# Kernel tuning notes

Measured on AMD Instinct MI355X. Metric: run time of the kernel, lower is better.

The kernel has to match this reference:

```python
import jax, jax.numpy as jnp
import numpy as np

B = 4
N0, N1, N2 = 32768, 8192, 2048
C0, C1, C2 = 256, 512, 1024
EPS = 1e-5  # torch BatchNorm1d default eps


def _mlp(x, w1, b1, g, be, w2, b2):
    # Linear -> BatchNorm1d (training-mode batch stats over B and N) -> ReLU -> Linear
    h = x @ w1 + b1                      # (B, N, H)
    mu = jnp.mean(h, axis=(0, 1))
    var = jnp.mean((h - mu) ** 2, axis=(0, 1))  # biased var, as torch BN uses for normalization
    h = jax.nn.relu((h - mu) * jax.lax.rsqrt(var + EPS) * g + be)
    return h @ w2 + b2


def _gather(feats, idx):
    # feats: (B, N_coarse, C), idx: (B, N_fine) -> (B, N_fine, C)
    return jax.vmap(lambda f, i: f[i])(feats, idx)


def _lin(key, fan_in, fan_out, scale=0.02):
    return jax.random.normal(key, (fan_in, fan_out), dtype=jnp.float32) * scale


def setup_inputs() -> dict:
    key = jax.random.key(0)
    ks = jax.random.split(key, 16)
    inp = {
        'f0': jax.random.normal(ks[0], (B, N0, C0), dtype=jnp.float32),
        'f1': jax.random.normal(ks[1], (B, N1, C1), dtype=jnp.float32),
        'f2': jax.random.normal(ks[2], (B, N2, C2), dtype=jnp.float32),
        # up_mlps[0]: MLP(C1, [C1, C0])
        'up0_w1': _lin(ks[3], C1, C1), 'up0_b1': jnp.zeros((C1,), jnp.float32),
        'up0_g': jnp.ones((C1,), jnp.float32), 'up0_be': jnp.zeros((C1,), jnp.float32),
        'up0_w2': _lin(ks[4], C1, C0), 'up0_b2': jnp.zeros((C0,), jnp.float32),
        # up_mlps[1]: MLP(C2, [C2, C1])
        'up1_w1': _lin(ks[5], C2, C2), 'up1_b1': jnp.zeros((C2,), jnp.float32),
        'up1_g': jnp.ones((C2,), jnp.float32), 'up1_be': jnp.zeros((C2,), jnp.float32),
        'up1_w2': _lin(ks[6], C2, C1), 'up1_b2': jnp.zeros((C1,), jnp.float32),
        # skip_mlps[0]: MLP(2*C0, [2*C0, C0])
        'skip0_w1': _lin(ks[7], 2 * C0, 2 * C0), 'skip0_b1': jnp.zeros((2 * C0,), jnp.float32),
        'skip0_g': jnp.ones((2 * C0,), jnp.float32), 'skip0_be': jnp.zeros((2 * C0,), jnp.float32),
        'skip0_w2': _lin(ks[8], 2 * C0, C0), 'skip0_b2': jnp.zeros((C0,), jnp.float32),
        # skip_mlps[1]: MLP(2*C1, [2*C1, C1])
        'skip1_w1': _lin(ks[9], 2 * C1, 2 * C1), 'skip1_b1': jnp.zeros((2 * C1,), jnp.float32),
        'skip1_g': jnp.ones((2 * C1,), jnp.float32), 'skip1_be': jnp.zeros((2 * C1,), jnp.float32),
        'skip1_w2': _lin(ks[10], 2 * C1, C1), 'skip1_b2': jnp.zeros((C1,), jnp.float32),
        'pool0': jax.random.randint(ks[11], (B, N0), 0, N1, dtype=jnp.int32),
        'pool1': jax.random.randint(ks[12], (B, N1), 0, N2, dtype=jnp.int32),
    }
    return inp


def reference(f0, f1, f2,
              up0_w1, up0_b1, up0_g, up0_be, up0_w2, up0_b2,
              up1_w1, up1_b1, up1_g, up1_be, up1_w2, up1_b2,
              skip0_w1, skip0_b1, skip0_g, skip0_be, skip0_w2, skip0_b2,
              skip1_w1, skip1_b1, skip1_g, skip1_be, skip1_w2, skip1_b2,
              pool0, pool1):
    # start at coarsest level
    x = f2                                               # (B, N2, C2)
    # level i = 1
    x = _mlp(x, up1_w1, up1_b1, up1_g, up1_be, up1_w2, up1_b2)   # (B, N2, C1)
    x = _gather(x, pool1)                                 # (B, N1, C1)
    x = _mlp(jnp.concatenate([f1, x], axis=-1),
             skip1_w1, skip1_b1, skip1_g, skip1_be, skip1_w2, skip1_b2)  # (B, N1, C1)
    # level i = 0
    x = _mlp(x, up0_w1, up0_b1, up0_g, up0_be, up0_w2, up0_b2)   # (B, N1, C0)
    x = _gather(x, pool0)                                 # (B, N0, C0)
    x = _mlp(jnp.concatenate([f0, x], axis=-1),
             skip0_w1, skip0_b1, skip0_g, skip0_be, skip0_w2, skip0_b2)  # (B, N0, C0)
    return x
```

## Files before the change

### kernel.cpp

```cpp
#include <hip/hip_runtime.h>


typedef unsigned short u16;
typedef __attribute__((ext_vector_type(8))) short bf16x8;
typedef __attribute__((ext_vector_type(4))) float f32x4;

#define UNROLL _Pragma("unroll")
#define EPW 264

__device__ __forceinline__ float b2f(u16 u) {
    union { unsigned int i; float f; } v; v.i = ((unsigned int)u) << 16; return v.f;
}
__device__ __forceinline__ u16 f2b(float f) {
    union { float f; unsigned int i; } v; v.f = f;
    unsigned int r = v.i + 0x7FFFu + ((v.i >> 16) & 1u);
    return (u16)(r >> 16);
}

__device__ __forceinline__ void gld_lds16(const u16* g, u16* l) {
    __builtin_amdgcn_global_load_lds(
        (const __attribute__((address_space(1))) unsigned int*)g,
        (__attribute__((address_space(3))) unsigned int*)l,
        16, 0, 0);
}

#define VMCNT(n) asm volatile("s_waitcnt vmcnt(" #n ")" ::: "memory")
#define LGKM0    asm volatile("s_waitcnt lgkmcnt(0)" ::: "memory")
#define BAR()    do{ asm volatile("" ::: "memory"); \
                     __builtin_amdgcn_s_barrier(); \
                     asm volatile("" ::: "memory"); }while(0)

union SMem {
    struct { u16 a[3][16384]; u16 b[16384]; } g;
    struct { u16 a[2][16384]; u16 b[2][16384]; float ss[2048]; } f;
    u16 ep[256 * EPW];
};

template <bool AFFINE_A, bool STATS, bool OUT_F32, bool GATHER>
__global__ __launch_bounds__(512, 2) void gemm_bn(
    const u16* __restrict__ A, const u16* __restrict__ BT, void* __restrict__ Cout,
    const float* __restrict__ scale, const float* __restrict__ shift,
    const float* __restrict__ bias,
    float* __restrict__ psum, float* __restrict__ psumsq,
    const u16* __restrict__ Xg, const int* __restrict__ pool,
    int nfShift, int Nc, int Chalf,
    int N, int K)
{
    __shared__ __align__(16) SMem sm;

    const int tid  = threadIdx.x;
    const int w    = tid >> 6;
    const int lane = tid & 63;
    const int wm   = w >> 2, wn = w & 3;
    const int l15  = lane & 15;
    const int xorv = (lane & 7) << 3;
    const int swz8 = ((lane & 7) ^ (lane >> 3)) << 3;
    const int kS0  = (((lane >> 4) << 3)) ^ xorv;
    const int kS1  = (32 + ((lane >> 4) << 3)) ^ xorv;

    int bm, bn;
    {
        const int nbn  = (int)gridDim.x;
        const int nwg  = nbn * (int)gridDim.y;
        const int flat = (int)(blockIdx.y * gridDim.x + blockIdx.x);
        const int wg   = (flat & 7) * (nwg >> 3) + (flat >> 3);
        const int lb   = 31 - __builtin_clz(nbn);
        bn = wg & (nbn - 1);
        bm = wg >> lb;
    }

    const u16* aS[2][2]; const u16* xS[2][2]; const u16* bS[2][2];
    int dA[2][2], dB[2][2], wIdx[2][2];
    UNROLL for (int u = 0; u < 2; u++)
    UNROLL for (int ld = 0; ld < 2; ld++) {
        const int urb = w * 16 + ld * 8;
        const int ur  = urb + (lane >> 3);
        {
            const int trb = urb + (urb >= 64 ? 64 : 0) + u * 64;
            const int tr  = ur  + (ur  >= 64 ? 64 : 0) + u * 64;
            dA[u][ld] = trb * 64;
            const int rowG = bm * 256 + tr;
            if constexpr (GATHER) {
                const int b = rowG >> nfShift;
                const int p = pool[rowG];
                aS[u][ld] = A  + (size_t)rowG * Chalf + swz8;
                xS[u][ld] = Xg + ((size_t)b * Nc + p) * Chalf + swz8;
            } else if constexpr (AFFINE_A) {
                aS[u][ld] = A + (size_t)rowG * K + ((lane & 7) << 3);
                wIdx[u][ld] = tr * 64 + swz8;
            } else {
                aS[u][ld] = A + (size_t)rowG * K + swz8;
            }
        }
        {
            const int trb = ((urb >> 5) << 6) + (urb & 31) + u * 32;
            const int tr  = ((ur  >> 5) << 6) + (ur  & 31) + u * 32;
            dB[u][ld] = trb * 64;
            bS[u][ld] = BT + (size_t)(bn * 256 + tr) * K + swz8;
        }
    }

    f32x4 acc[8][4];
    const f32x4 zero = {0.f, 0.f, 0.f, 0.f};
    UNROLL for (int i = 0; i < 8; i++)
    UNROLL for (int j = 0; j < 4; j++) acc[i][j] = zero;
    bf16x8 afr[4][2];
    bf16x8 bfr[2][2][2];
    uint4 rA[2][2];

#define GLD_B(u, BASE, KOF) do{ \
    u16* bt_ = (BASE); \
    gld_lds16(bS[u][0] + (KOF), bt_ + dB[u][0]); \
    gld_lds16(bS[u][1] + (KOF), bt_ + dB[u][1]); }while(0)

#define ISSUE_A(u, BASE, KOF) do{ \
    u16* at_ = (BASE); \
    if constexpr (GATHER) { \
        const u16 *s0_, *s1_; \
        if ((KOF) < Chalf) { s0_ = aS[u][0] + (KOF); s1_ = aS[u][1] + (KOF); } \
        else { s0_ = xS[u][0] + ((KOF) - Chalf); s1_ = xS[u][1] + ((KOF) - Chalf); } \
        gld_lds16(s0_, at_ + dA[u][0]); \
        gld_lds16(s1_, at_ + dA[u][1]); \
    } else { \
        gld_lds16(aS[u][0] + (KOF), at_ + dA[u][0]); \
        gld_lds16(aS[u][1] + (KOF), at_ + dA[u][1]); \
    } }while(0)

#define LOAD_RA(u, KOF) do{ \
    rA[u][0] = *(const uint4*)(aS[u][0] + (KOF)); \
    rA[u][1] = *(const uint4*)(aS[u][1] + (KOF)); }while(0)

#define AFFW(u, BASE, KOF) do{ if constexpr (AFFINE_A) { \
    u16* at_ = (BASE); \
    const int kb_ = (KOF) + ((lane & 7) << 3); \
    const float4 sc0_ = *(const float4*)&sm.f.ss[kb_]; \
    const float4 sc1_ = *(const float4*)&sm.f.ss[kb_ + 4]; \
    const float4 sh0_ = *(const float4*)&sm.f.ss[1024 + kb_]; \
    const float4 sh1_ = *(const float4*)&sm.f.ss[1024 + kb_ + 4]; \
    UNROLL for (int ld_ = 0; ld_ < 2; ld_++) { \
        union { uint4 u4; u16 s[8]; } r_, o_; r_.u4 = rA[u][ld_]; \
        o_.s[0] = f2b(fmaxf(b2f(r_.s[0]) * sc0_.x + sh0_.x, 0.f)); \
        o_.s[1] = f2b(fmaxf(b2f(r_.s[1]) * sc0_.y + sh0_.y, 0.f)); \
        o_.s[2] = f2b(fmaxf(b2f(r_.s[2]) * sc0_.z + sh0_.z, 0.f)); \
        o_.s[3] = f2b(fmaxf(b2f(r_.s[3]) * sc0_.w + sh0_.w, 0.f)); \
        o_.s[4] = f2b(fmaxf(b2f(r_.s[4]) * sc1_.x + sh1_.x, 0.f)); \
        o_.s[5] = f2b(fmaxf(b2f(r_.s[5]) * sc1_.y + sh1_.y, 0.f)); \
        o_.s[6] = f2b(fmaxf(b2f(r_.s[6]) * sc1_.z + sh1_.z, 0.f)); \
        o_.s[7] = f2b(fmaxf(b2f(r_.s[7]) * sc1_.w + sh1_.w, 0.f)); \
        *(uint4*)&at_[wIdx[u][ld_]] = o_.u4; } \
    LGKM0; } }while(0)

#define READ_A(base, qi) do{ const u16* p_ = (base); \
    UNROLL for (int i_ = 0; i_ < 4; i_++) { \
        const int rb_ = (wm * 128 + ((qi) * 4 + i_) * 16 + l15) * 64; \
        afr[i_][0] = *(const bf16x8*)&p_[rb_ + kS0]; \
        afr[i_][1] = *(const bf16x8*)&p_[rb_ + kS1]; } }while(0)

#define READ_B(base, qj) do{ const u16* p_ = (base); \
    UNROLL for (int j_ = 0; j_ < 2; j_++) { \
        const int rb_ = (wn * 64 + ((qj) * 2 + j_) * 16 + l15) * 64; \
        bfr[qj][j_][0] = *(const bf16x8*)&p_[rb_ + kS0]; \
        bfr[qj][j_][1] = *(const bf16x8*)&p_[rb_ + kS1]; } }while(0)

#define MFMA_Q(qi, qj) do{ __builtin_amdgcn_s_setprio(1); \
    UNROLL for (int i_ = 0; i_ < 4; i_++) \
    UNROLL for (int j_ = 0; j_ < 2; j_++) { \
        acc[(qi)*4+i_][(qj)*2+j_] = __builtin_amdgcn_mfma_f32_16x16x32_bf16( \
            afr[i_][0], bfr[qj][j_][0], acc[(qi)*4+i_][(qj)*2+j_], 0, 0, 0); \
        acc[(qi)*4+i_][(qj)*2+j_] = __builtin_amdgcn_mfma_f32_16x16x32_bf16( \
            afr[i_][1], bfr[qj][j_][1], acc[(qi)*4+i_][(qj)*2+j_], 0, 0, 0); } \
    __builtin_amdgcn_s_setprio(0); }while(0)

    const int nkt = K >> 6;

    if constexpr (AFFINE_A) {
        for (int i = tid; i < K; i += 512) {
            sm.f.ss[i] = scale[i]; sm.f.ss[1024 + i] = shift[i];
        }
        LOAD_RA(0, 0);
        GLD_B(0, &sm.f.b[0][0], 0); GLD_B(1, &sm.f.b[0][0], 0);
        LOAD_RA(1, 0);
        asm volatile("s_waitcnt vmcnt(0) lgkmcnt(0)" ::: "memory");
        BAR();
        AFFW(0, &sm.f.a[0][0], 0);
        BAR();

        for (int t = 0; t < nkt - 1; ++t) {
            const int buf = t & 1, nb = buf ^ 1;
            const int kofN = (t + 1) << 6;
            u16* aB = &sm.f.a[buf][0]; u16* aN = &sm.f.a[nb][0];
            u16* bB = &sm.f.b[buf][0]; u16* bN = &sm.f.b[nb][0];
            LOAD_RA(0, kofN);
            READ_A(aB, 0); READ_B(bB, 0);
            BAR();
            MFMA_Q(0, 0);
            GLD_B(0, bN, kofN);
            VMCNT(6); BAR();
            READ_B(bB, 1);
            MFMA_Q(0, 1);
            GLD_B(1, bN, kofN);
            VMCNT(6);
            AFFW(1, aB, t << 6);
            BAR();
            READ_A(aB, 1);
            MFMA_Q(1, 1);
            LOAD_RA(1, kofN);
            MFMA_Q(1, 0);
            VMCNT(4);
            AFFW(0, aN, kofN);
            BAR();
        }
        {
            const int t = nkt - 1, buf = t & 1;
            u16* aB = &sm.f.a[buf][0]; u16* bB = &sm.f.b[buf][0];
            READ_A(aB, 0); READ_B(bB, 0);
            BAR();
            MFMA_Q(0, 0);
            VMCNT(2); BAR();
            READ_B(bB, 1);
            MFMA_Q(0, 1);
            VMCNT(0);
            AFFW(1, aB, t << 6);
            BAR();
            READ_A(aB, 1);
            MFMA_Q(1, 1);
            BAR();
            MFMA_Q(1, 0);
        }
    } else {
        u16* const bb = &sm.g.b[0];
        GLD_B(0, bb, 0); GLD_B(1, bb, 0);
        ISSUE_A(0, &sm.g.a[0][0], 0);  ISSUE_A(1, &sm.g.a[0][0], 0);
        ISSUE_A(0, &sm.g.a[1][0], 64); ISSUE_A(1, &sm.g.a[1][0], 64);
        VMCNT(0); BAR();

        int rs = 0;
        for (int t = 0; t < nkt - 2; ++t) {
            const int ws = (rs == 0) ? 2 : rs - 1;
            const int kofB = (t + 1) << 6, kofL = (t + 2) << 6;
            const u16* aR = &sm.g.a[0][0] + rs * 16384;
            u16* aW = &sm.g.a[0][0] + ws * 16384;
            READ_A(aR, 0); READ_B(bb, 0);
            LGKM0; VMCNT(4); BAR();
            GLD_B(0, bb, kofB);
            MFMA_Q(0, 0);
            READ_B(bb, 1);
            LGKM0; BAR();
            GLD_B(1, bb, kofB);
            MFMA_Q(0, 1);
            READ_A(aR, 1);
            ISSUE_A(0, aW, kofL);
            BAR();
            MFMA_Q(1, 1);
            ISSUE_A(1, aW, kofL);
            MFMA_Q(1, 0);
            VMCNT(6); BAR();
            rs = (rs == 2) ? 0 : rs + 1;
        }
        {
            const int t = nkt - 2;
            const int kofB = (t + 1) << 6;
            const u16* aR = &sm.g.a[0][0] + rs * 16384;
            READ_A(aR, 0); READ_B(bb, 0);
            LGKM0; VMCNT(4); BAR();
            GLD_B(0, bb, kofB);
            MFMA_Q(0, 0);
            READ_B(bb, 1);
            LGKM0; BAR();
            GLD_B(1, bb, kofB);
            MFMA_Q(0, 1);
            READ_A(aR, 1);
            BAR();
            MFMA_Q(1, 1);
            MFMA_Q(1, 0);
            VMCNT(2); BAR();
            rs = (rs == 2) ? 0 : rs + 1;
        }
        {
            const u16* aR = &sm.g.a[0][0] + rs * 16384;
            READ_A(aR, 0); READ_B(bb, 0);
            VMCNT(0); BAR();
            MFMA_Q(0, 0);
            READ_B(bb, 1);
            MFMA_Q(0, 1);
            READ_A(aR, 1);
            MFMA_Q(1, 1);
            MFMA_Q(1, 0);
            LGKM0; BAR();
        }
    }

    const int cl = l15, quad = lane >> 4;
    if constexpr (OUT_F32) {
        UNROLL for (int j = 0; j < 4; j++) {
            const int col = bn * 256 + wn * 64 + j * 16 + cl;
            const float bcol = bias[col];
            UNROLL for (int i = 0; i < 8; i++) {
                const int r0 = bm * 256 + wm * 128 + i * 16 + quad * 4;
                UNROLL for (int r = 0; r < 4; r++)
                    ((float*)Cout)[(size_t)(r0 + r) * N + col] = acc[i][j][r] + bcol;
            }
        }
    } else {
        UNROLL for (int j = 0; j < 4; j++) {
            const int colL = wn * 64 + j * 16 + cl;
            const int col = bn * 256 + colL;
            float bcol = 0.f;
            if constexpr (!STATS) bcol = bias[col];
            float s = 0.f, ss2 = 0.f;
            UNROLL for (int i = 0; i < 8; i++) {
                const int rL0 = wm * 128 + i * 16 + quad * 4;
                UNROLL for (int r = 0; r < 4; r++) {
                    const float v = acc[i][j][r];
                    if constexpr (STATS) { s += v; ss2 += v * v; }
                    sm.ep[(rL0 + r) * EPW + colL] = f2b(v + bcol);
                }
            }
            if constexpr (STATS) {
                s   += __shfl_xor(s, 16);   s   += __shfl_xor(s, 32);
                ss2 += __shfl_xor(ss2, 16); ss2 += __shfl_xor(ss2, 32);
                if (quad == 0) { atomicAdd(&psum[col], s); atomicAdd(&psumsq[col], ss2); }
            }
        }
        __syncthreads();
        u16* Cb = (u16*)Cout;
        UNROLL for (int it = 0; it < 16; it++) {
            const int row = it * 16 + (tid >> 5);
            const int c8  = (tid & 31) * 8;
            const uint4 v = *(const uint4*)&sm.ep[row * EPW + c8];
            *(uint4*)(Cb + (size_t)(bm * 256 + row) * N + bn * 256 + c8) = v;
        }
    }
#undef GLD_B
#undef ISSUE_A
#undef LOAD_RA
#undef AFFW
#undef READ_A
#undef READ_B
#undef MFMA_Q
}

__global__ void cvt_transpose_w(const float* __restrict__ W, u16* __restrict__ WT, int K, int N) {
    __shared__ float t[32][33];
    const int tx = threadIdx.x, ty = threadIdx.y;
    const int n0 = blockIdx.x * 32, k0 = blockIdx.y * 32;
#pragma unroll
    for (int r = 0; r < 4; r++)
        t[ty + r * 8][tx] = W[(size_t)(k0 + ty + r * 8) * N + n0 + tx];
    __syncthreads();
#pragma unroll
    for (int r = 0; r < 4; r++)
        WT[(size_t)(n0 + ty + r * 8) * K + k0 + tx] = f2b(t[tx][ty + r * 8]);
}

__global__ void cvt_f32_bf16(const float* __restrict__ x, u16* __restrict__ y, long n8) {
    const long t = (long)blockIdx.x * 256 + threadIdx.x;
    if (t >= n8) return;
    const float4 a = ((const float4*)x)[t * 2];
    const float4 b = ((const float4*)x)[t * 2 + 1];
    union { uint4 u; u16 s[8]; } o;
    o.s[0] = f2b(a.x); o.s[1] = f2b(a.y); o.s[2] = f2b(a.z); o.s[3] = f2b(a.w);
    o.s[4] = f2b(b.x); o.s[5] = f2b(b.y); o.s[6] = f2b(b.z); o.s[7] = f2b(b.w);
    ((uint4*)y)[t] = o.u;
}

__global__ void bn_finalize(const float* __restrict__ sum, const float* __restrict__ sumsq,
                            const float* __restrict__ g, const float* __restrict__ be,
                            float* __restrict__ scale, float* __restrict__ shift,
                            int Cc, float invM) {
    const int c = blockIdx.x * 256 + threadIdx.x;
    if (c >= Cc) return;
    const float mu = sum[c] * invM;
    const float var = fmaf(sumsq[c], invM, -mu * mu);
    const float sc = g[c] * rsqrtf(var + 1e-5f);
    scale[c] = sc;
    shift[c] = fmaf(-mu, sc, be[c]);
}

extern "C" void kernel_launch(void* const* d_in, const int* in_sizes, int n_in,
                              void* d_out, int out_size, void* d_ws, size_t ws_size,
                              hipStream_t stream) {
    const float* f0     = (const float*)d_in[0];
    const float* f1     = (const float*)d_in[1];
    const float* f2     = (const float*)d_in[2];
    const float* up0_w1 = (const float*)d_in[3];
    const float* up0_g  = (const float*)d_in[5];
    const float* up0_be = (const float*)d_in[6];
    const float* up0_w2 = (const float*)d_in[7];
    const float* up0_b2 = (const float*)d_in[8];
    const float* up1_w1 = (const float*)d_in[9];
    const float* up1_g  = (const float*)d_in[11];
    const float* up1_be = (const float*)d_in[12];
    const float* up1_w2 = (const float*)d_in[13];
    const float* up1_b2 = (const float*)d_in[14];
    const float* sk0_w1 = (const float*)d_in[15];
    const float* sk0_g  = (const float*)d_in[17];
    const float* sk0_be = (const float*)d_in[18];
    const float* sk0_w2 = (const float*)d_in[19];
    const float* sk0_b2 = (const float*)d_in[20];
    const float* sk1_w1 = (const float*)d_in[21];
    const float* sk1_g  = (const float*)d_in[23];
    const float* sk1_be = (const float*)d_in[24];
    const float* sk1_w2 = (const float*)d_in[25];
    const float* sk1_b2 = (const float*)d_in[26];
    const int* pool0    = (const int*)d_in[27];
    const int* pool1    = (const int*)d_in[28];
    float* out = (float*)d_out;

    char* ws = (char*)d_ws;
    size_t off = 0;
    auto alloc = [&](size_t bytes) -> void* {
        void* p = ws + off;
        off += (bytes + 255) & ~(size_t)255;
        return p;
    };
    u16* w_up1_1 = (u16*)alloc((size_t)1024 * 1024 * 2);
    u16* w_up1_2 = (u16*)alloc((size_t)512 * 1024 * 2);
    u16* w_sk1_1 = (u16*)alloc((size_t)1024 * 1024 * 2);
    u16* w_sk1_2 = (u16*)alloc((size_t)512 * 1024 * 2);
    u16* w_up0_1 = (u16*)alloc((size_t)512 * 512 * 2);
    u16* w_up0_2 = (u16*)alloc((size_t)256 * 512 * 2);
    u16* w_sk0_1 = (u16*)alloc((size_t)512 * 512 * 2);
    u16* w_sk0_2 = (u16*)alloc((size_t)256 * 512 * 2);
    float* stats = (float*)alloc((size_t)4 * 4096 * 4);
    u16* Hbuf    = (u16*)alloc((size_t)131072 * 512 * 2);
    u16* Xbuf    = (u16*)alloc((size_t)32768 * 512 * 2);
    u16* f0b     = (u16*)alloc((size_t)4 * 32768 * 256 * 2);
    u16* f1b     = (u16*)alloc((size_t)4 * 8192 * 512 * 2);
    u16* f2b_    = (u16*)alloc((size_t)4 * 2048 * 1024 * 2);

    const dim3 tb(32, 8);
    cvt_transpose_w<<<dim3(32, 32), tb, 0, stream>>>(up1_w1, w_up1_1, 1024, 1024);
    cvt_transpose_w<<<dim3(16, 32), tb, 0, stream>>>(up1_w2, w_up1_2, 1024, 512);
    cvt_transpose_w<<<dim3(32, 32), tb, 0, stream>>>(sk1_w1, w_sk1_1, 1024, 1024);
    cvt_transpose_w<<<dim3(16, 32), tb, 0, stream>>>(sk1_w2, w_sk1_2, 1024, 512);
    cvt_transpose_w<<<dim3(16, 16), tb, 0, stream>>>(up0_w1, w_up0_1, 512, 512);
    cvt_transpose_w<<<dim3(8, 16),  tb, 0, stream>>>(up0_w2, w_up0_2, 512, 256);
    cvt_transpose_w<<<dim3(16, 16), tb, 0, stream>>>(sk0_w1, w_sk0_1, 512, 512);
    cvt_transpose_w<<<dim3(8, 16),  tb, 0, stream>>>(sk0_w2, w_sk0_2, 512, 256);

    hipMemsetAsync(stats, 0, (size_t)4 * 4096 * sizeof(float), stream);
    cvt_f32_bf16<<<4096,  256, 0, stream>>>(f2, f2b_, 8388608L / 8);
    cvt_f32_bf16<<<8192,  256, 0, stream>>>(f1, f1b, 16777216L / 8);
    cvt_f32_bf16<<<16384, 256, 0, stream>>>(f0, f0b, 33554432L / 8);

    float* st0 = stats;
    float* st1 = stats + 4096;
    float* st2 = stats + 8192;
    float* st3 = stats + 12288;

    gemm_bn<false, true, false, false><<<dim3(4, 32), 512, 0, stream>>>(
        f2b_, w_up1_1, Hbuf, nullptr, nullptr, nullptr, st0, st0 + 1024,
        nullptr, nullptr, 0, 0, 0, 1024, 1024);
    bn_finalize<<<4, 256, 0, stream>>>(st0, st0 + 1024, up1_g, up1_be, st0 + 2048, st0 + 3072, 1024, 1.f / 8192.f);
    gemm_bn<true, false, false, false><<<dim3(2, 32), 512, 0, stream>>>(
        Hbuf, w_up1_2, Xbuf, st0 + 2048, st0 + 3072, up1_b2, nullptr, nullptr,
        nullptr, nullptr, 0, 0, 0, 512, 1024);

    gemm_bn<false, true, false, true><<<dim3(4, 128), 512, 0, stream>>>(
        f1b, w_sk1_1, Hbuf, nullptr, nullptr, nullptr, st1, st1 + 1024,
        Xbuf, pool1, 13, 2048, 512, 1024, 1024);
    bn_finalize<<<4, 256, 0, stream>>>(st1, st1 + 1024, sk1_g, sk1_be, st1 + 2048, st1 + 3072, 1024, 1.f / 32768.f);
    gemm_bn<true, false, false, false><<<dim3(2, 128), 512, 0, stream>>>(
        Hbuf, w_sk1_2, Xbuf, st1 + 2048, st1 + 3072, sk1_b2, nullptr, nullptr,
        nullptr, nullptr, 0, 0, 0, 512, 1024);

    gemm_bn<false, true, false, false><<<dim3(2, 128), 512, 0, stream>>>(
        Xbuf, w_up0_1, Hbuf, nullptr, nullptr, nullptr, st2, st2 + 1024,
        nullptr, nullptr, 0, 0, 0, 512, 512);
    bn_finalize<<<2, 256, 0, stream>>>(st2, st2 + 1024, up0_g, up0_be, st2 + 2048, st2 + 3072, 512, 1.f / 32768.f);
    gemm_bn<true, false, false, false><<<dim3(1, 128), 512, 0, stream>>>(
        Hbuf, w_up0_2, Xbuf, st2 + 2048, st2 + 3072, up0_b2, nullptr, nullptr,
        nullptr, nullptr, 0, 0, 0, 256, 512);

    gemm_bn<false, true, false, true><<<dim3(2, 512), 512, 0, stream>>>(
        f0b, w_sk0_1, Hbuf, nullptr, nullptr, nullptr, st3, st3 + 1024,
        Xbuf, pool0, 15, 8192, 256, 512, 512);
    bn_finalize<<<2, 256, 0, stream>>>(st3, st3 + 1024, sk0_g, sk0_be, st3 + 2048, st3 + 3072, 512, 1.f / 131072.f);
    gemm_bn<true, false, true, false><<<dim3(1, 512), 512, 0, stream>>>(
        Hbuf, w_sk0_2, out, st3 + 2048, st3 + 3072, sk0_b2, nullptr, nullptr,
        nullptr, nullptr, 0, 0, 0, 256, 512);
}
```

Measured before the change: 833.4 us.

## Shrink GEMM tile to 256x128 with 1024-thread blocks and double-buffered B

Blocks now cover a 256x128 output tile with 16 waves of 64x32 each instead of 256x256 with 8 waves, and launch 1024 threads with double the grid along N. B tiles become double-buffered at half size and the K-loop pipeline is restructured into two MFMA phases per step. The aim is more blocks and waves to hide latency and better CU fill on the small-N GEMMs. The cost is lower arithmetic intensity per tile, more redundant A traffic and more barriers per K-step. Launch bounds (1024,4) also cap registers hard.

Result: slower. 850.8 us (+2.1%).

```diff
diff --git a/kernel.cpp b/kernel.cpp
--- a/kernel.cpp
+++ b/kernel.cpp
@@ -6,7 +6,7 @@
 typedef __attribute__((ext_vector_type(4))) float f32x4;
 
 #define UNROLL _Pragma("unroll")
-#define EPW 264
+#define EPW 136
 
 __device__ __forceinline__ float b2f(u16 u) {
     union { unsigned int i; float f; } v; v.i = ((unsigned int)u) << 16; return v.f;
@@ -31,13 +31,13 @@
                      asm volatile("" ::: "memory"); }while(0)
 
 union SMem {
-    struct { u16 a[3][16384]; u16 b[16384]; } g;
-    struct { u16 a[2][16384]; u16 b[2][16384]; float ss[2048]; } f;
+    struct { u16 a[3][16384]; u16 b[2][8192]; } g;
+    struct { u16 a[2][16384]; u16 b[2][8192]; float ss[2048]; } f;
     u16 ep[256 * EPW];
 };
 
 template <bool AFFINE_A, bool STATS, bool OUT_F32, bool GATHER>
-__global__ __launch_bounds__(512, 2) void gemm_bn(
+__global__ __launch_bounds__(1024, 4) void gemm_bn(
     const u16* __restrict__ A, const u16* __restrict__ BT, void* __restrict__ Cout,
     const float* __restrict__ scale, const float* __restrict__ shift,
     const float* __restrict__ bias,
@@ -55,7 +55,7 @@
     const int l15  = lane & 15;
     const int xorv = (lane & 7) << 3;
     const int swz8 = ((lane & 7) ^ (lane >> 3)) << 3;
-    const int kS0  = (((lane >> 4) << 3)) ^ xorv;
+    const int kS0  = ((lane >> 4) << 3) ^ xorv;
     const int kS1  = (32 + ((lane >> 4) << 3)) ^ xorv;
 
     int bm, bn;
@@ -69,247 +69,219 @@
         bm = wg >> lb;
     }
 
-    const u16* aS[2][2]; const u16* xS[2][2]; const u16* bS[2][2];
-    int dA[2][2], dB[2][2], wIdx[2][2];
-    UNROLL for (int u = 0; u < 2; u++)
-    UNROLL for (int ld = 0; ld < 2; ld++) {
-        const int urb = w * 16 + ld * 8;
-        const int ur  = urb + (lane >> 3);
-        {
-            const int trb = urb + (urb >= 64 ? 64 : 0) + u * 64;
-            const int tr  = ur  + (ur  >= 64 ? 64 : 0) + u * 64;
-            dA[u][ld] = trb * 64;
-            const int rowG = bm * 256 + tr;
-            if constexpr (GATHER) {
-                const int b = rowG >> nfShift;
-                const int p = pool[rowG];
-                aS[u][ld] = A  + (size_t)rowG * Chalf + swz8;
-                xS[u][ld] = Xg + ((size_t)b * Nc + p) * Chalf + swz8;
-            } else if constexpr (AFFINE_A) {
-                aS[u][ld] = A + (size_t)rowG * K + ((lane & 7) << 3);
-                wIdx[u][ld] = tr * 64 + swz8;
-            } else {
-                aS[u][ld] = A + (size_t)rowG * K + swz8;
-            }
-        }
-        {
-            const int trb = ((urb >> 5) << 6) + (urb & 31) + u * 32;
-            const int tr  = ((ur  >> 5) << 6) + (ur  & 31) + u * 32;
-            dB[u][ld] = trb * 64;
-            bS[u][ld] = BT + (size_t)(bn * 256 + tr) * K + swz8;
+    const u16* aS[2]; const u16* xS[2]; const u16* bSp;
+    int dA[2], dB, wIdx[2];
+    UNROLL for (int u = 0; u < 2; u++) {
+        const int trb = (w >> 2) * 64 + (w & 3) * 8 + u * 32;
+        const int tr  = trb + (lane >> 3);
+        dA[u] = trb * 64;
+        const int rowG = bm * 256 + tr;
+        if constexpr (GATHER) {
+            const int b = rowG >> nfShift;
+            const int p = pool[rowG];
+            aS[u] = A  + (size_t)rowG * Chalf + swz8;
+            xS[u] = Xg + ((size_t)b * Nc + p) * Chalf + swz8;
+        } else if constexpr (AFFINE_A) {
+            aS[u] = A + (size_t)rowG * K + ((lane & 7) << 3);
+            wIdx[u] = tr * 64 + swz8;
+        } else {
+            aS[u] = A + (size_t)rowG * K + swz8;
         }
     }
-
-    f32x4 acc[8][4];
+    {
+        const int trb = w * 8;
+        dB = trb * 64;
+        bSp = BT + (size_t)(bn * 128 + trb + (lane >> 3)) * K + swz8;
+    }
+
+    f32x4 acc[4][2];
     const f32x4 zero = {0.f, 0.f, 0.f, 0.f};
-    UNROLL for (int i = 0; i < 8; i++)
-    UNROLL for (int j = 0; j < 4; j++) acc[i][j] = zero;
-    bf16x8 afr[4][2];
-    bf16x8 bfr[2][2][2];
-    uint4 rA[2][2];
-
-#define GLD_B(u, BASE, KOF) do{ \
-    u16* bt_ = (BASE); \
-    gld_lds16(bS[u][0] + (KOF), bt_ + dB[u][0]); \
-    gld_lds16(bS[u][1] + (KOF), bt_ + dB[u][1]); }while(0)
+    UNROLL for (int i = 0; i < 4; i++)
+    UNROLL for (int j = 0; j < 2; j++) acc[i][j] = zero;
+    bf16x8 afr[2][2];
+    bf16x8 bfr[2][2];
+    uint4 rA[2];
+
+#define GLD_B(BASE, KOF) gld_lds16(bSp + (KOF), (BASE) + dB)
 
 #define ISSUE_A(u, BASE, KOF) do{ \
-    u16* at_ = (BASE); \
     if constexpr (GATHER) { \
-        const u16 *s0_, *s1_; \
-        if ((KOF) < Chalf) { s0_ = aS[u][0] + (KOF); s1_ = aS[u][1] + (KOF); } \
-        else { s0_ = xS[u][0] + ((KOF) - Chalf); s1_ = xS[u][1] + ((KOF) - Chalf); } \
-        gld_lds16(s0_, at_ + dA[u][0]); \
-        gld_lds16(s1_, at_ + dA[u][1]); \
+        const u16* s_ = ((KOF) < Chalf) ? (aS[u] + (KOF)) : (xS[u] + ((KOF) - Chalf)); \
+        gld_lds16(s_, (BASE) + dA[u]); \
     } else { \
-        gld_lds16(aS[u][0] + (KOF), at_ + dA[u][0]); \
-        gld_lds16(aS[u][1] + (KOF), at_ + dA[u][1]); \
+        gld_lds16(aS[u] + (KOF), (BASE) + dA[u]); \
     } }while(0)
 
-#define LOAD_RA(u, KOF) do{ \
-    rA[u][0] = *(const uint4*)(aS[u][0] + (KOF)); \
-    rA[u][1] = *(const uint4*)(aS[u][1] + (KOF)); }while(0)
+#define LOAD_RA(u, KOF) do{ rA[u] = *(const uint4*)(aS[u] + (KOF)); }while(0)
 
 #define AFFW(u, BASE, KOF) do{ if constexpr (AFFINE_A) { \
-    u16* at_ = (BASE); \
     const int kb_ = (KOF) + ((lane & 7) << 3); \
     const float4 sc0_ = *(const float4*)&sm.f.ss[kb_]; \
     const float4 sc1_ = *(const float4*)&sm.f.ss[kb_ + 4]; \
     const float4 sh0_ = *(const float4*)&sm.f.ss[1024 + kb_]; \
     const float4 sh1_ = *(const float4*)&sm.f.ss[1024 + kb_ + 4]; \
-    UNROLL for (int ld_ = 0; ld_ < 2; ld_++) { \
-        union { uint4 u4; u16 s[8]; } r_, o_; r_.u4 = rA[u][ld_]; \
-        o_.s[0] = f2b(fmaxf(b2f(r_.s[0]) * sc0_.x + sh0_.x, 0.f)); \
-        o_.s[1] = f2b(fmaxf(b2f(r_.s[1]) * sc0_.y + sh0_.y, 0.f)); \
-        o_.s[2] = f2b(fmaxf(b2f(r_.s[2]) * sc0_.z + sh0_.z, 0.f)); \
-        o_.s[3] = f2b(fmaxf(b2f(r_.s[3]) * sc0_.w + sh0_.w, 0.f)); \
-        o_.s[4] = f2b(fmaxf(b2f(r_.s[4]) * sc1_.x + sh1_.x, 0.f)); \
-        o_.s[5] = f2b(fmaxf(b2f(r_.s[5]) * sc1_.y + sh1_.y, 0.f)); \
-        o_.s[6] = f2b(fmaxf(b2f(r_.s[6]) * sc1_.z + sh1_.z, 0.f)); \
-        o_.s[7] = f2b(fmaxf(b2f(r_.s[7]) * sc1_.w + sh1_.w, 0.f)); \
-        *(uint4*)&at_[wIdx[u][ld_]] = o_.u4; } \
+    union { uint4 u4; u16 s[8]; } r_, o_; r_.u4 = rA[u]; \
+    o_.s[0] = f2b(fmaxf(b2f(r_.s[0]) * sc0_.x + sh0_.x, 0.f)); \
+    o_.s[1] = f2b(fmaxf(b2f(r_.s[1]) * sc0_.y + sh0_.y, 0.f)); \
+    o_.s[2] = f2b(fmaxf(b2f(r_.s[2]) * sc0_.z + sh0_.z, 0.f)); \
+    o_.s[3] = f2b(fmaxf(b2f(r_.s[3]) * sc0_.w + sh0_.w, 0.f)); \
+    o_.s[4] = f2b(fmaxf(b2f(r_.s[4]) * sc1_.x + sh1_.x, 0.f)); \
+    o_.s[5] = f2b(fmaxf(b2f(r_.s[5]) * sc1_.y + sh1_.y, 0.f)); \
+    o_.s[6] = f2b(fmaxf(b2f(r_.s[6]) * sc1_.z + sh1_.z, 0.f)); \
+    o_.s[7] = f2b(fmaxf(b2f(r_.s[7]) * sc1_.w + sh1_.w, 0.f)); \
+    *(uint4*)&((BASE))[wIdx[u]] = o_.u4; \
     LGKM0; } }while(0)
 
 #define READ_A(base, qi) do{ const u16* p_ = (base); \
-    UNROLL for (int i_ = 0; i_ < 4; i_++) { \
-        const int rb_ = (wm * 128 + ((qi) * 4 + i_) * 16 + l15) * 64; \
-        afr[i_][0] = *(const bf16x8*)&p_[rb_ + kS0]; \
-        afr[i_][1] = *(const bf16x8*)&p_[rb_ + kS1]; } }while(0)
-
-#define READ_B(base, qj) do{ const u16* p_ = (base); \
+    UNROLL for (int i2 = 0; i2 < 2; i2++) { \
+        const int rb_ = (wm * 64 + ((qi) * 2 + i2) * 16 + l15) * 64; \
+        afr[i2][0] = *(const bf16x8*)&p_[rb_ + kS0]; \
+        afr[i2][1] = *(const bf16x8*)&p_[rb_ + kS1]; } }while(0)
+
+#define READ_B(base) do{ const u16* p_ = (base); \
     UNROLL for (int j_ = 0; j_ < 2; j_++) { \
-        const int rb_ = (wn * 64 + ((qj) * 2 + j_) * 16 + l15) * 64; \
-        bfr[qj][j_][0] = *(const bf16x8*)&p_[rb_ + kS0]; \
-        bfr[qj][j_][1] = *(const bf16x8*)&p_[rb_ + kS1]; } }while(0)
-
-#define MFMA_Q(qi, qj) do{ __builtin_amdgcn_s_setprio(1); \
-    UNROLL for (int i_ = 0; i_ < 4; i_++) \
+        const int rb_ = (wn * 32 + j_ * 16 + l15) * 64; \
+        bfr[j_][0] = *(const bf16x8*)&p_[rb_ + kS0]; \
+        bfr[j_][1] = *(const bf16x8*)&p_[rb_ + kS1]; } }while(0)
+
+#define MFMA_PH(qi) do{ __builtin_amdgcn_s_setprio(1); \
+    UNROLL for (int i2 = 0; i2 < 2; i2++) \
     UNROLL for (int j_ = 0; j_ < 2; j_++) { \
-        acc[(qi)*4+i_][(qj)*2+j_] = __builtin_amdgcn_mfma_f32_16x16x32_bf16( \
-            afr[i_][0], bfr[qj][j_][0], acc[(qi)*4+i_][(qj)*2+j_], 0, 0, 0); \
-        acc[(qi)*4+i_][(qj)*2+j_] = __builtin_amdgcn_mfma_f32_16x16x32_bf16( \
-            afr[i_][1], bfr[qj][j_][1], acc[(qi)*4+i_][(qj)*2+j_], 0, 0, 0); } \
+        acc[(qi)*2+i2][j_] = __builtin_amdgcn_mfma_f32_16x16x32_bf16( \
+            afr[i2][0], bfr[j_][0], acc[(qi)*2+i2][j_], 0, 0, 0); \
+        acc[(qi)*2+i2][j_] = __builtin_amdgcn_mfma_f32_16x16x32_bf16( \
+            afr[i2][1], bfr[j_][1], acc[(qi)*2+i2][j_], 0, 0, 0); } \
     __builtin_amdgcn_s_setprio(0); }while(0)
 
     const int nkt = K >> 6;
 
     if constexpr (AFFINE_A) {
-        for (int i = tid; i < K; i += 512) {
+        for (int i = tid; i < K; i += 1024) {
             sm.f.ss[i] = scale[i]; sm.f.ss[1024 + i] = shift[i];
         }
-        LOAD_RA(0, 0);
-        GLD_B(0, &sm.f.b[0][0], 0); GLD_B(1, &sm.f.b[0][0], 0);
-        LOAD_RA(1, 0);
-        asm volatile("s_waitcnt vmcnt(0) lgkmcnt(0)" ::: "memory");
+        LOAD_RA(0, 0); LOAD_RA(1, 0);
+        GLD_B(&sm.f.b[0][0], 0);
+        GLD_B(&sm.f.b[1][0], 64);
+        LGKM0;
         BAR();
         AFFW(0, &sm.f.a[0][0], 0);
+        LOAD_RA(0, 64);
+        VMCNT(2);
         BAR();
 
-        for (int t = 0; t < nkt - 1; ++t) {
-            const int buf = t & 1, nb = buf ^ 1;
+        for (int t = 0; t < nkt - 2; ++t) {
+            u16* aB = &sm.f.a[t & 1][0]; u16* aN = &sm.f.a[(t + 1) & 1][0];
+            u16* bR = &sm.f.b[t & 1][0];
+            const int kofN = (t + 1) << 6, kof2 = (t + 2) << 6;
+            AFFW(1, aB, t << 6);
+            LOAD_RA(1, kofN);
+            READ_A(aB, 0); READ_B(bR);
+            LGKM0; BAR();
+            MFMA_PH(0);
+            AFFW(0, aN, kofN);
+            LOAD_RA(0, kof2);
+            GLD_B(bR, kof2);
+            READ_A(aB, 1);
+            LGKM0; VMCNT(3);
+            BAR();
+            MFMA_PH(1);
+        }
+        {
+            const int t = nkt - 2;
+            u16* aB = &sm.f.a[t & 1][0]; u16* aN = &sm.f.a[(t + 1) & 1][0];
+            u16* bR = &sm.f.b[t & 1][0];
             const int kofN = (t + 1) << 6;
-            u16* aB = &sm.f.a[buf][0]; u16* aN = &sm.f.a[nb][0];
-            u16* bB = &sm.f.b[buf][0]; u16* bN = &sm.f.b[nb][0];
-            LOAD_RA(0, kofN);
-            READ_A(aB, 0); READ_B(bB, 0);
+            AFFW(1, aB, t << 6); LOAD_RA(1, kofN);
+            READ_A(aB, 0); READ_B(bR);
+            LGKM0; BAR();
+            MFMA_PH(0);
+            AFFW(0, aN, kofN);
+            READ_A(aB, 1);
+            LGKM0; VMCNT(1);
             BAR();
-            MFMA_Q(0, 0);
-            GLD_B(0, bN, kofN);
-            VMCNT(6); BAR();
-            READ_B(bB, 1);
-            MFMA_Q(0, 1);
-            GLD_B(1, bN, kofN);
-            VMCNT(6);
+            MFMA_PH(1);
+        }
+        {
+            const int t = nkt - 1;
+            u16* aB = &sm.f.a[t & 1][0]; u16* bR = &sm.f.b[t & 1][0];
             AFFW(1, aB, t << 6);
-            BAR();
+            READ_A(aB, 0); READ_B(bR);
+            LGKM0; BAR();
+            MFMA_PH(0);
             READ_A(aB, 1);
-            MFMA_Q(1, 1);
-            LOAD_RA(1, kofN);
-            MFMA_Q(1, 0);
-            VMCNT(4);
-            AFFW(0, aN, kofN);
-            BAR();
-        }
-        {
-            const int t = nkt - 1, buf = t & 1;
-            u16* aB = &sm.f.a[buf][0]; u16* bB = &sm.f.b[buf][0];
-            READ_A(aB, 0); READ_B(bB, 0);
-            BAR();
-            MFMA_Q(0, 0);
-            VMCNT(2); BAR();
-            READ_B(bB, 1);
-            MFMA_Q(0, 1);
-            VMCNT(0);
-            AFFW(1, aB, t << 6);
-            BAR();
-            READ_A(aB, 1);
-            MFMA_Q(1, 1);
-            BAR();
-            MFMA_Q(1, 0);
+            LGKM0; BAR();
+            MFMA_PH(1);
         }
     } else {
-        u16* const bb = &sm.g.b[0];
-        GLD_B(0, bb, 0); GLD_B(1, bb, 0);
+        GLD_B(&sm.g.b[0][0], 0);
+        GLD_B(&sm.g.b[1][0], 64);
         ISSUE_A(0, &sm.g.a[0][0], 0);  ISSUE_A(1, &sm.g.a[0][0], 0);
         ISSUE_A(0, &sm.g.a[1][0], 64); ISSUE_A(1, &sm.g.a[1][0], 64);
         VMCNT(0); BAR();
 
         int rs = 0;
         for (int t = 0; t < nkt - 2; ++t) {
-            const int ws = (rs == 0) ? 2 : rs - 1;
-            const int kofB = (t + 1) << 6, kofL = (t + 2) << 6;
-            const u16* aR = &sm.g.a[0][0] + rs * 16384;
+            const int ws = (rs >= 1) ? rs - 1 : 2;
+            u16* aR = &sm.g.a[0][0] + rs * 16384;
             u16* aW = &sm.g.a[0][0] + ws * 16384;
-            READ_A(aR, 0); READ_B(bb, 0);
-            LGKM0; VMCNT(4); BAR();
-            GLD_B(0, bb, kofB);
-            MFMA_Q(0, 0);
-            READ_B(bb, 1);
-            LGKM0; BAR();
-            GLD_B(1, bb, kofB);
-            MFMA_Q(0, 1);
+            u16* bR = &sm.g.b[t & 1][0];
+            const int kof2 = (t + 2) << 6;
+            ISSUE_A(0, aW, kof2);
+            READ_A(aR, 0); READ_B(bR);
+            LGKM0; BAR();
+            MFMA_PH(0);
+            ISSUE_A(1, aW, kof2);
+            GLD_B(bR, kof2);
             READ_A(aR, 1);
-            ISSUE_A(0, aW, kofL);
+            LGKM0; VMCNT(3);
             BAR();
-            MFMA_Q(1, 1);
-            ISSUE_A(1, aW, kofL);
-            MFMA_Q(1, 0);
-            VMCNT(6); BAR();
+            MFMA_PH(1);
             rs = (rs == 2) ? 0 : rs + 1;
         }
         {
-            const int t = nkt - 2;
-            const int kofB = (t + 1) << 6;
-            const u16* aR = &sm.g.a[0][0] + rs * 16384;
-            READ_A(aR, 0); READ_B(bb, 0);
-            LGKM0; VMCNT(4); BAR();
-            GLD_B(0, bb, kofB);
-            MFMA_Q(0, 0);
-            READ_B(bb, 1);
-            LGKM0; BAR();
-            GLD_B(1, bb, kofB);
-            MFMA_Q(0, 1);
+            u16* aR = &sm.g.a[0][0] + rs * 16384;
+            u16* bR = &sm.g.b[(nkt - 2) & 1][0];
+            READ_A(aR, 0); READ_B(bR);
+            LGKM0; BAR();
+            MFMA_PH(0);
             READ_A(aR, 1);
+            LGKM0; VMCNT(0);
             BAR();
-            MFMA_Q(1, 1);
-            MFMA_Q(1, 0);
-            VMCNT(2); BAR();
+            MFMA_PH(1);
             rs = (rs == 2) ? 0 : rs + 1;
         }
         {
-            const u16* aR = &sm.g.a[0][0] + rs * 16384;
-            READ_A(aR, 0); READ_B(bb, 0);
-            VMCNT(0); BAR();
-            MFMA_Q(0, 0);
-            READ_B(bb, 1);
-            MFMA_Q(0, 1);
+            u16* aR = &sm.g.a[0][0] + rs * 16384;
+            u16* bR = &sm.g.b[(nkt - 1) & 1][0];
+            READ_A(aR, 0); READ_B(bR);
+            LGKM0; BAR();
+            MFMA_PH(0);
             READ_A(aR, 1);
-            MFMA_Q(1, 1);
-            MFMA_Q(1, 0);
-            LGKM0; BAR();
+            LGKM0; BAR();
+            MFMA_PH(1);
         }
     }
 
     const int cl = l15, quad = lane >> 4;
     if constexpr (OUT_F32) {
-        UNROLL for (int j = 0; j < 4; j++) {
-            const int col = bn * 256 + wn * 64 + j * 16 + cl;
+        UNROLL for (int j = 0; j < 2; j++) {
+            const int col = bn * 128 + wn * 32 + j * 16 + cl;
             const float bcol = bias[col];
-            UNROLL for (int i = 0; i < 8; i++) {
-                const int r0 = bm * 256 + wm * 128 + i * 16 + quad * 4;
+            UNROLL for (int i = 0; i < 4; i++) {
+                const int r0 = bm * 256 + wm * 64 + i * 16 + quad * 4;
                 UNROLL for (int r = 0; r < 4; r++)
                     ((float*)Cout)[(size_t)(r0 + r) * N + col] = acc[i][j][r] + bcol;
             }
         }
     } else {
-        UNROLL for (int j = 0; j < 4; j++) {
-            const int colL = wn * 64 + j * 16 + cl;
-            const int col = bn * 256 + colL;
+        UNROLL for (int j = 0; j < 2; j++) {
+            const int colL = wn * 32 + j * 16 + cl;
+            const int col = bn * 128 + colL;
             float bcol = 0.f;
             if constexpr (!STATS) bcol = bias[col];
             float s = 0.f, ss2 = 0.f;
-            UNROLL for (int i = 0; i < 8; i++) {
-                const int rL0 = wm * 128 + i * 16 + quad * 4;
+            UNROLL for (int i = 0; i < 4; i++) {
+                const int rL0 = wm * 64 + i * 16 + quad * 4;
                 UNROLL for (int r = 0; r < 4; r++) {
                     const float v = acc[i][j][r];
                     if constexpr (STATS) { s += v; ss2 += v * v; }
@@ -324,11 +296,11 @@
         }
         __syncthreads();
         u16* Cb = (u16*)Cout;
-        UNROLL for (int it = 0; it < 16; it++) {
-            const int row = it * 16 + (tid >> 5);
-            const int c8  = (tid & 31) * 8;
+        UNROLL for (int it = 0; it < 4; it++) {
+            const int row = it * 64 + (tid >> 4);
+            const int c8  = (tid & 15) * 8;
             const uint4 v = *(const uint4*)&sm.ep[row * EPW + c8];
-            *(uint4*)(Cb + (size_t)(bm * 256 + row) * N + bn * 256 + c8) = v;
+            *(uint4*)(Cb + (size_t)(bm * 256 + row) * N + bn * 128 + c8) = v;
         }
     }
 #undef GLD_B
@@ -337,7 +309,7 @@
 #undef AFFW
 #undef READ_A
 #undef READ_B
-#undef MFMA_Q
+#undef MFMA_PH
 }
 
 __global__ void cvt_transpose_w(const float* __restrict__ W, u16* __restrict__ WT, int K, int N) {
@@ -449,35 +421,35 @@
     float* st2 = stats + 8192;
     float* st3 = stats + 12288;
 
-    gemm_bn<false, true, false, false><<<dim3(4, 32), 512, 0, stream>>>(
+    gemm_bn<false, true, false, false><<<dim3(8, 32), 1024, 0, stream>>>(
         f2b_, w_up1_1, Hbuf, nullptr, nullptr, nullptr, st0, st0 + 1024,
         nullptr, nullptr, 0, 0, 0, 1024, 1024);
     bn_finalize<<<4, 256, 0, stream>>>(st0, st0 + 1024, up1_g, up1_be, st0 + 2048, st0 + 3072, 1024, 1.f / 8192.f);
-    gemm_bn<true, false, false, false><<<dim3(2, 32), 512, 0, stream>>>(
+    gemm_bn<true, false, false, false><<<dim3(4, 32), 1024, 0, stream>>>(
         Hbuf, w_up1_2, Xbuf, st0 + 2048, st0 + 3072, up1_b2, nullptr, nullptr,
         nullptr, nullptr, 0, 0, 0, 512, 1024);
 
-    gemm_bn<false, true, false, true><<<dim3(4, 128), 512, 0, stream>>>(
+    gemm_bn<false, true, false, true><<<dim3(8, 128), 1024, 0, stream>>>(
         f1b, w_sk1_1, Hbuf, nullptr, nullptr, nullptr, st1, st1 + 1024,
         Xbuf, pool1, 13, 2048, 512, 1024, 1024);
     bn_finalize<<<4, 256, 0, stream>>>(st1, st1 + 1024, sk1_g, sk1_be, st1 + 2048, st1 + 3072, 1024, 1.f / 32768.f);
-    gemm_bn<true, false, false, false><<<dim3(2, 128), 512, 0, stream>>>(
+    gemm_bn<true, false, false, false><<<dim3(4, 128), 1024, 0, stream>>>(
         Hbuf, w_sk1_2, Xbuf, st1 + 2048, st1 + 3072, sk1_b2, nullptr, nullptr,
         nullptr, nullptr, 0, 0, 0, 512, 1024);
 
-    gemm_bn<false, true, false, false><<<dim3(2, 128), 512, 0, stream>>>(
+    gemm_bn<false, true, false, false><<<dim3(4, 128), 1024, 0, stream>>>(
         Xbuf, w_up0_1, Hbuf, nullptr, nullptr, nullptr, st2, st2 + 1024,
         nullptr, nullptr, 0, 0, 0, 512, 512);
     bn_finalize<<<2, 256, 0, stream>>>(st2, st2 + 1024, up0_g, up0_be, st2 + 2048, st2 + 3072, 512, 1.f / 32768.f);
-    gemm_bn<true, false, false, false><<<dim3(1, 128), 512, 0, stream>>>(
+    gemm_bn<true, false, false, false><<<dim3(2, 128), 1024, 0, stream>>>(
         Hbuf, w_up0_2, Xbuf, st2 + 2048, st2 + 3072, up0_b2, nullptr, nullptr,
         nullptr, nullptr, 0, 0, 0, 256, 512);
 
-    gemm_bn<false, true, false, true><<<dim3(2, 512), 512, 0, stream>>>(
+    gemm_bn<false, true, false, true><<<dim3(4, 512), 1024, 0, stream>>>(
         f0b, w_sk0_1, Hbuf, nullptr, nullptr, nullptr, st3, st3 + 1024,
         Xbuf, pool0, 15, 8192, 256, 512, 512);
     bn_finalize<<<2, 256, 0, stream>>>(st3, st3 + 1024, sk0_g, sk0_be, st3 + 2048, st3 + 3072, 512, 1.f / 131072.f);
-    gemm_bn<true, false, true, false><<<dim3(1, 512), 512, 0, stream>>>(
+    gemm_bn<true, false, true, false><<<dim3(2, 512), 1024, 0, stream>>>(
         Hbuf, w_sk0_2, out, st3 + 2048, st3 + 3072, sk0_b2, nullptr, nullptr,
         nullptr, nullptr, 0, 0, 0, 256, 512);
 }
```
